# Kernel tuning notes

Measured on AMD Instinct MI355X. Metric: run time of the kernel, lower is better.

## Reference

```python
import jax, jax.numpy as jnp
import numpy as np
from jax import lax

D_MODEL = 200
N_LAYER = 12
NHEADS = 8
HEADDIM = 50
D_STATE = 64
D_INNER = 2 * D_MODEL            # 400
CONV_DIM = D_INNER + 2 * D_STATE  # 528 (ngroups=1)
D_IN_PROJ = 2 * D_INNER + 2 * D_STATE + NHEADS  # 936
D_CONV = 4
EPS = 1e-5


def rmsnorm(x, w):
    v = jnp.mean(jnp.square(x), axis=-1, keepdims=True)
    return x * lax.rsqrt(v + EPS) * w


def groupnorm(x, groups, g, b):
    B, C, H, W = x.shape
    xg = x.reshape(B, groups, C // groups, H, W)
    mu = jnp.mean(xg, axis=(2, 3, 4), keepdims=True)
    var = jnp.mean(jnp.square(xg - mu), axis=(2, 3, 4), keepdims=True)
    xn = ((xg - mu) * lax.rsqrt(var + EPS)).reshape(B, C, H, W)
    return xn * g[:, None, None] + b[:, None, None]


def patch_embed(x, pe_conv_w, proj_in_w, gn_g, gn_b, spec_w):
    b, c, l, d = x.shape
    # time path: 'b c l d' -> (b, 1, c*l, d), conv -> (b, 25, c*l, 8)
    time_x = x.reshape(b, 1, c * l, d)
    t = lax.conv_general_dilated(time_x, proj_in_w, (1, 25), ((0, 0), (24, 24)),
                                 dimension_numbers=('NCHW', 'OIHW', 'NCHW'))
    t = jax.nn.gelu(groupnorm(t, 5, gn_g, gn_b), approximate=False)
    time_emb = t.transpose(0, 2, 1, 3).reshape(b, c, l, D_MODEL)
    # freq path: rfft over patch dim, norm='forward'
    spec = jnp.abs(jnp.fft.rfft(x, axis=-1, norm='forward'))  # (b,c,l,101)
    spec_emb = jnp.einsum('bclf,df->bcld', spec, spec_w)
    patch = time_emb + spec_emb
    # depthwise 7x7 positional conv over (d, c, l)
    pos = lax.conv_general_dilated(patch.transpose(0, 3, 1, 2), pe_conv_w, (1, 1),
                                   ((3, 3), (3, 3)),
                                   dimension_numbers=('NCHW', 'OIHW', 'NCHW'),
                                   feature_group_count=D_MODEL)
    return patch + pos.transpose(0, 2, 3, 1)


def ssd_scan(xh, dt, B, C, A, D):
    # xh: (b,l,h,p)  dt: (b,l,h)  B,C: (b,l,n)  A,D: (h,)
    b, l, h, p = xh.shape

    def step(state, inp):
        x_t, dt_t, B_t, C_t = inp
        dA = jnp.exp(dt_t * A)  # (b,h)
        state = state * dA[:, :, None, None] + \
            (dt_t[:, :, None, None] * x_t[:, :, :, None]) * B_t[:, None, None, :]
        y = jnp.einsum('bhpn,bn->bhp', state, C_t)
        return state, y

    state0 = jnp.zeros((b, h, p, D_STATE), xh.dtype)
    _, ys = lax.scan(step, state0,
                     (xh.transpose(1, 0, 2, 3), dt.transpose(1, 0, 2),
                      B.transpose(1, 0, 2), C.transpose(1, 0, 2)))
    return ys.transpose(1, 0, 2, 3) + xh * D[None, None, :, None]


def mamba2(u, in_w, conv_w, conv_b, dt_bias, A_log, D, gn_w, out_w):
    b, l, _ = u.shape
    zxbcdt = u @ in_w.T  # (b,l,936)
    z = zxbcdt[..., :D_INNER]
    xBC = zxbcdt[..., D_INNER:D_INNER + CONV_DIM]
    dt = jax.nn.softplus(zxbcdt[..., D_INNER + CONV_DIM:] + dt_bias)  # (b,l,8)
    # causal depthwise conv1d, kernel 4
    xc = lax.conv_general_dilated(xBC.transpose(0, 2, 1), conv_w, (1,), ((D_CONV - 1, 0),),
                                  dimension_numbers=('NCH', 'OIH', 'NCH'),
                                  feature_group_count=CONV_DIM)
    xBC = jax.nn.silu((xc + conv_b[:, None]).transpose(0, 2, 1))
    x = xBC[..., :D_INNER].reshape(b, l, NHEADS, HEADDIM)
    Bm = xBC[..., D_INNER:D_INNER + D_STATE]
    Cm = xBC[..., D_INNER + D_STATE:]
    y = ssd_scan(x, dt, Bm, Cm, -jnp.exp(A_log), D).reshape(b, l, D_INNER)
    y = rmsnorm(y * jax.nn.silu(z), gn_w)  # RMSNormGated, norm_before_gate=False
    return y @ out_w.T


@jax.checkpoint
def layer(hidden, residual, norm_w, in_w, conv_w, conv_b, dt_bias, A_log, D, gn_w, out_w):
    residual = hidden + residual
    hidden = mamba2(rmsnorm(residual, norm_w), in_w, conv_w, conv_b, dt_bias, A_log, D, gn_w, out_w)
    return hidden, residual


def forward(x, pe_conv_w, proj_in_w, gn_g, gn_b, spec_w, norm_w, in_proj_w, conv_w, conv_b,
            dt_bias, A_log, D, gnorm_w, out_proj_w, norm_f_w, head_w, head_b):
    b, c, l, d = x.shape
    hidden = patch_embed(x, pe_conv_w, proj_in_w, gn_g, gn_b, spec_w).reshape(b, c * l, d)
    residual = jnp.zeros_like(hidden)
    for i in range(N_LAYER):
        hidden, residual = layer(hidden, residual, norm_w[i], in_proj_w[i], conv_w[i],
                                 conv_b[i], dt_bias[i], A_log[i], D[i], gnorm_w[i], out_proj_w[i])
    hidden = rmsnorm(hidden + residual, norm_f_w).reshape(b, c, l, d)
    return hidden @ head_w.T + head_b


def setup_inputs():
    key = jax.random.key(0)
    ks = jax.random.split(key, 12)
    B, CH, L, P = 16, 19, 30, 200

    def g(k, shape, scale):
        return jax.random.normal(k, shape, jnp.float32) * scale

    dt = jax.random.uniform(ks[8], (N_LAYER, NHEADS), jnp.float32, 1e-3, 0.1)
    return {
        'x': g(ks[0], (B, CH, L, P), 1.0),
        'pe_conv_w': g(ks[1], (D_MODEL, 1, 7, 7), 0.15),
        'proj_in_w': g(ks[2], (25, 1, 1, 49), 0.14),
        'gn_g': jnp.ones(25, jnp.float32),
        'gn_b': jnp.zeros(25, jnp.float32),
        'spec_w': g(ks[3], (D_MODEL, 101), 0.1),
        'norm_w': jnp.ones((N_LAYER, D_MODEL), jnp.float32),
        'in_proj_w': g(ks[4], (N_LAYER, D_IN_PROJ, D_MODEL), 0.07),
        'conv_w': g(ks[5], (N_LAYER, CONV_DIM, 1, D_CONV), 0.4),
        'conv_b': jnp.zeros((N_LAYER, CONV_DIM), jnp.float32),
        'dt_bias': jnp.log(jnp.expm1(dt)),
        'A_log': jnp.log(jax.random.uniform(ks[9], (N_LAYER, NHEADS), jnp.float32, 1.0, 16.0)),
        'D': jnp.ones((N_LAYER, NHEADS), jnp.float32),
        'gnorm_w': jnp.ones((N_LAYER, D_INNER), jnp.float32),
        'out_proj_w': g(ks[6], (N_LAYER, D_MODEL, D_INNER), 0.05),
        'norm_f_w': jnp.ones(D_MODEL, jnp.float32),
        'head_w': g(ks[7], (D_MODEL, D_MODEL), 0.07),
        'head_b': jnp.zeros(D_MODEL, jnp.float32),
    }


def reference(x, pe_conv_w, proj_in_w, gn_g, gn_b, spec_w, norm_w, in_proj_w, conv_w, conv_b,
              dt_bias, A_log, D, gnorm_w, out_proj_w, norm_f_w, head_w, head_b):
    return forward(x, pe_conv_w, proj_in_w, gn_g, gn_b, spec_w, norm_w, in_proj_w, conv_w,
                   conv_b, dt_bias, A_log, D, gnorm_w, out_proj_w, norm_f_w, head_w, head_b)
```

## Files before the change

### kernel.cpp

```cpp
#include <hip/hip_runtime.h>
#include <hip/hip_bf16.h>
#include <math.h>

#define D_MODEL   200
#define N_LAYER   12
#define NHEADS    8
#define HEADDIM   50
#define D_STATE   64
#define D_INNER   400
#define CONV_DIM  528
#define D_IN_PROJ 936
#define D_CONV    4
#define EPS       1e-5f

#define BATCH 16
#define CH    19
#define LLEN  30
#define SEQ   570
#define NTOK  9120
#define NFREQ 101

typedef __attribute__((ext_vector_type(8))) short s8v;
typedef __attribute__((ext_vector_type(4))) float f32x4;

// ... 418 lines not shown
        dtb[(size_t)m * NHEADS + h] = (raw > 20.f) ? raw : log1pf(expf(raw));
    }
}

__global__ __launch_bounds__(256) void dt_gemv_kernel(
    const float* __restrict__ u, const float* __restrict__ Win,
    const float* __restrict__ dt_bias, float* __restrict__ dtb, int layer)
{
    int tid = threadIdx.x;
    int tok = blockIdx.x * 4 + (tid >> 6);
    int head = (tid >> 3) & 7;
    int l8 = tid & 7;
    const float* ur = u + (size_t)tok * 200;
    const float* wr = Win + (size_t)layer * D_IN_PROJ * 200 + (size_t)(928 + head) * 200;
    float s = 0.f;
    for (int k = l8; k < 200; k += 8) s = fmaf(ur[k], wr[k], s);
    s += __shfl_xor(s, 1, 64);
    s += __shfl_xor(s, 2, 64);
    s += __shfl_xor(s, 4, 64);
    if (l8 == 0) {
        float raw = s + dt_bias[layer * NHEADS + head];
        dtb[(size_t)tok * NHEADS + head] = (raw > 20.f) ? raw : log1pf(expf(raw));
    }
}

__global__ __launch_bounds__(256) void dtconv2_kernel(
    const float* __restrict__ zxbcdt, const float* __restrict__ cw,
    const float* __restrict__ cb, float* __restrict__ xBC, int layer)
{
    int b = blockIdx.x, tt = blockIdx.y;
    int t0 = tt * 8;
    __shared__ float zs[11][528];
    const float* cwl = cw + (size_t)layer * CONV_DIM * 4;
    const float* cbl = cb + (size_t)layer * CONV_DIM;
    for (int i = threadIdx.x; i < 11 * 528; i += 256) {
        int r = i / 528, ch = i - r * 528;
        int t = t0 - 3 + r;
        zs[r][ch] = (t >= 0 && t < SEQ)
                        ? zxbcdt[(size_t)(b * SEQ + t) * D_IN_PROJ + D_INNER + ch] : 0.f;
    }
    __syncthreads();
    for (int o = threadIdx.x; o < 8 * 528; o += 256) {
        int tr = o / 528, ch = o - tr * 528;
        int t = t0 + tr;
        if (t >= SEQ) continue;
        float acc = cbl[ch];
#pragma unroll
        for (int k = 0; k < 4; k++)
            acc = fmaf(zs[tr + k][ch], cwl[ch * 4 + k], acc);
        xBC[(size_t)(b * SEQ + t) * CONV_DIM + ch] = acc / (1.f + __expf(-acc));
    }
}

__global__ __launch_bounds__(256) void ssd_state7_kernel(
    const float* __restrict__ xBC, const float* __restrict__ dtb,
    const float* __restrict__ A_log, float* __restrict__ Sbuf,
    float* __restrict__ Pd, int layer, int lchunk, int nchunk)
{
    int b = blockIdx.x, c = blockIdx.y, bz = blockIdx.z;
    int tid = threadIdx.x;
    int hl = tid >> 6, p = tid & 63;
    int h = bz * 4 + hl;
    float A = -expf(A_log[layer * NHEADS + h]);

    __shared__ __align__(16) float sB[4][2][128];
    int t0 = c * lchunk;
    int npairs = lchunk >> 1;

    const float* xb  = xBC + (size_t)(b * SEQ + t0) * CONV_DIM;
    const float* dtp = dtb + (size_t)(b * SEQ + t0) * NHEADS + h;

    int ldtok = (p >> 4) & 1;
    int ldf4  = 100 + (p & 15);
    int ldoff = ldtok * 64 + ((p & 15) << 2);

    float4 gv;
    if (p < 32) {
        gv = ((const float4*)(xb + (size_t)ldtok * CONV_DIM))[ldf4];
        *(float4*)&sB[hl][0][ldoff] = gv;
    }
    float nx0 = (p < HEADDIM) ? xb[h * HEADDIM + p] : 0.f;
    float nx1 = (p < HEADDIM) ? xb[CONV_DIM + h * HEADDIM + p] : 0.f;
    float ndt0 = dtp[0];
    float ndt1 = dtp[NHEADS];
    if (npairs > 1 && p < 32)
        gv = ((const float4*)(xb + (size_t)(2 + ldtok) * CONV_DIM))[ldf4];

    float s[64];
#pragma unroll
    for (int n = 0; n < 64; n++) s[n] = 0.f;
    float pacc = 1.f;

    for (int i = 0; i < npairs; i++) {
        int buf = i & 1;
        float x0 = nx0, x1 = nx1, dt0 = ndt0, dt1 = ndt1;
        if (i + 1 < npairs) {
            if (p < 32) *(float4*)&sB[hl][buf ^ 1][ldoff] = gv;
            const float* xn = xb + (size_t)(2 * (i + 1)) * CONV_DIM;
            nx0 = (p < HEADDIM) ? xn[h * HEADDIM + p] : 0.f;
            nx1 = (p < HEADDIM) ? xn[CONV_DIM + h * HEADDIM + p] : 0.f;
            ndt0 = dtp[(size_t)(2 * (i + 1)) * NHEADS];
            ndt1 = dtp[(size_t)(2 * (i + 1) + 1) * NHEADS];
            if (i + 2 < npairs && p < 32)
                gv = ((const float4*)(xb + (size_t)(2 * (i + 2) + ldtok) * CONV_DIM))[ldf4];
        }
#pragma unroll
        for (int k = 0; k < 2; k++) {
            float dtv = k ? dt1 : dt0;
            float xp  = k ? x1 : x0;
            float dA = __expf(dtv * A);
            float u  = dtv * xp;
            pacc *= dA;
            const float4* B4 = (const float4*)&sB[hl][buf][k * 64];
#pragma unroll
            for (int n4 = 0; n4 < 16; n4++) {
                float4 bq = B4[n4];
                s[4 * n4 + 0] = fmaf(s[4 * n4 + 0], dA, u * bq.x);
                s[4 * n4 + 1] = fmaf(s[4 * n4 + 1], dA, u * bq.y);
                s[4 * n4 + 2] = fmaf(s[4 * n4 + 2], dA, u * bq.z);
                s[4 * n4 + 3] = fmaf(s[4 * n4 + 3], dA, u * bq.w);
            }
        }
    }

    if (p < HEADDIM) {
        float* Sb = Sbuf + ((size_t)((b * NHEADS + h) * nchunk + c)) * (HEADDIM * 64)
                    + p * 64;
#pragma unroll
        for (int n4 = 0; n4 < 16; n4++)
            ((float4*)Sb)[n4] = make_float4(s[4 * n4], s[4 * n4 + 1],
                                            s[4 * n4 + 2], s[4 * n4 + 3]);
    }
    if (p == 0) Pd[(b * NHEADS + h) * nchunk + c] = pacc;
}

__global__ __launch_bounds__(512) void ssd_state_kernel(
    const float* __restrict__ xBC, const float* __restrict__ dtb,
    const float* __restrict__ A_log, float* __restrict__ Sbuf,
    float* __restrict__ Pd, int layer, int lchunk, int nchunk)
{
    int b = blockIdx.x, c = blockIdx.y;
    int tid = threadIdx.x;
    int h = tid >> 6, p = tid & 63;
    float A = -expf(A_log[layer * NHEADS + h]);

    __shared__ float sh[2][544];
    int t0 = c * lchunk, tend = t0 + lchunk;

    {
        const float* base = xBC + (size_t)(b * SEQ + t0) * CONV_DIM;
        sh[0][tid] = base[tid];
        if (tid < 24) {
            int e2 = 512 + tid;
            sh[0][e2] = (e2 < 528) ? base[e2]
                                   : dtb[(size_t)(b * SEQ + t0) * NHEADS + (e2 - 528)];
        }
    }
    __syncthreads();

    float s[64];
#pragma unroll
    for (int n = 0; n < 64; n++) s[n] = 0.f;
    float pacc = 1.f;

    for (int t = t0; t < tend; t++) {
        int cur = (t - t0) & 1, nxt = cur ^ 1;
        float pf0 = 0.f, pf1 = 0.f;
        if (t + 1 < tend) {
            const float* base = xBC + (size_t)(b * SEQ + t + 1) * CONV_DIM;
            pf0 = base[tid];
            if (tid < 24) {
                int e2 = 512 + tid;
                pf1 = (e2 < 528) ? base[e2]
                                 : dtb[(size_t)(b * SEQ + t + 1) * NHEADS + (e2 - 528)];
            }
        }
        float dtv = sh[cur][528 + h];
        float xp  = (p < HEADDIM) ? sh[cur][h * HEADDIM + p] : 0.f;
        float dA = __expf(dtv * A);
        float u  = dtv * xp;
        pacc *= dA;
        const float4* B4 = (const float4*)&sh[cur][D_INNER];
#pragma unroll
        for (int n4 = 0; n4 < 16; n4++) {
            float4 bq = B4[n4];
            s[4 * n4 + 0] = fmaf(s[4 * n4 + 0], dA, u * bq.x);
            s[4 * n4 + 1] = fmaf(s[4 * n4 + 1], dA, u * bq.y);
            s[4 * n4 + 2] = fmaf(s[4 * n4 + 2], dA, u * bq.z);
            s[4 * n4 + 3] = fmaf(s[4 * n4 + 3], dA, u * bq.w);
        }
        if (t + 1 < tend) {
            sh[nxt][tid] = pf0;
            if (tid < 24) sh[nxt][512 + tid] = pf1;
        }
        __syncthreads();
    }

    if (p < HEADDIM) {
        float* Sb = Sbuf + ((size_t)((b * NHEADS + h) * nchunk + c)) * (HEADDIM * 64)
                    + p * 64;
#pragma unroll
        for (int n4 = 0; n4 < 16; n4++)
            ((float4*)Sb)[n4] = make_float4(s[4 * n4], s[4 * n4 + 1],
                                            s[4 * n4 + 2], s[4 * n4 + 3]);
    }
    if (p == 0) Pd[(b * NHEADS + h) * nchunk + c] = pacc;
}

__global__ __launch_bounds__(256) void ssd_scan2b_kernel(
    float* __restrict__ Sbuf, const float* __restrict__ Pd, int nchunk)
{
    int bh = blockIdx.x;
    int e = blockIdx.y * 256 + threadIdx.x;
    if (e >= HEADDIM * 64) return;
    float* base = Sbuf + (size_t)bh * nchunk * (HEADDIM * 64) + e;
    const float* pd = Pd + bh * nchunk;
    float cur = 0.f;
    for (int c = 0; c < nchunk; c++) {
        float l = base[(size_t)c * (HEADDIM * 64)];
        base[(size_t)c * (HEADDIM * 64)] = cur;
        cur = fmaf(pd[c], cur, l);
    }
}

__global__ __launch_bounds__(256) void ssd_out7_kernel(
    const float* __restrict__ xBC, const float* __restrict__ dtb,
    const float* __restrict__ zxbcdt, const float* __restrict__ A_log,
    const float* __restrict__ Dv, const float* __restrict__ Sbuf,
    const float* __restrict__ gw, short* __restrict__ ybf,
    float* __restrict__ ssq, int layer, int lchunk, int nchunk)
{
    int b = blockIdx.x, c = blockIdx.y, bz = blockIdx.z;
    int tid = threadIdx.x;
    int hl = tid >> 6, p = tid & 63;
    int h = bz * 4 + hl;
    float A = -expf(A_log[layer * NHEADS + h]);
    float Dh = Dv[layer * NHEADS + h];
    float gval = (p < HEADDIM) ? gw[(size_t)layer * D_INNER + h * HEADDIM + p] : 0.f;

    __shared__ __align__(16) float sBC[4][2][256];
    int t0 = c * lchunk;
    int npairs = lchunk >> 1;

    const float* xb  = xBC + (size_t)(b * SEQ + t0) * CONV_DIM;
    const float* zb  = zxbcdt + (size_t)(b * SEQ + t0) * D_IN_PROJ;
    const float* dtp = dtb + (size_t)(b * SEQ + t0) * NHEADS + h;

    int ldtok = p >> 5;
    int ldf4  = 100 + (p & 31);
    int ldoff = ldtok * 128 + ((p & 31) << 2);

    float4 gv;
    gv = ((const float4*)(xb + (size_t)ldtok * CONV_DIM))[ldf4];
    *(float4*)&sBC[hl][0][ldoff] = gv;
    float nx0 = (p < HEADDIM) ? xb[h * HEADDIM + p] : 0.f;
    float nx1 = (p < HEADDIM) ? xb[CONV_DIM + h * HEADDIM + p] : 0.f;
    float nz0 = (p < HEADDIM) ? zb[h * HEADDIM + p] : 0.f;
    float nz1 = (p < HEADDIM) ? zb[D_IN_PROJ + h * HEADDIM + p] : 0.f;
    float ndt0 = dtp[0];
    float ndt1 = dtp[NHEADS];
    if (npairs > 1)
        gv = ((const float4*)(xb + (size_t)(2 + ldtok) * CONV_DIM))[ldf4];

    float s[64];
    if (p < HEADDIM) {
        const float* Sb = Sbuf + ((size_t)((b * NHEADS + h) * nchunk + c)) * (HEADDIM * 64)
                          + p * 64;
#pragma unroll
        for (int n4 = 0; n4 < 16; n4++) {
            float4 v = ((const float4*)Sb)[n4];
            s[4 * n4] = v.x; s[4 * n4 + 1] = v.y; s[4 * n4 + 2] = v.z; s[4 * n4 + 3] = v.w;
        }
    } else {
#pragma unroll
        for (int n = 0; n < 64; n++) s[n] = 0.f;
    }

    for (int i = 0; i < npairs; i++) {
        int buf = i & 1;
        int t = t0 + 2 * i;
        float x0 = nx0, x1 = nx1, z0 = nz0, z1 = nz1, dt0 = ndt0, dt1 = ndt1;
        if (i + 1 < npairs) {
            *(float4*)&sBC[hl][buf ^ 1][ldoff] = gv;
            const float* xn = xb + (size_t)(2 * (i + 1)) * CONV_DIM;
            const float* zn = zb + (size_t)(2 * (i + 1)) * D_IN_PROJ;
            nx0 = (p < HEADDIM) ? xn[h * HEADDIM + p] : 0.f;
            nx1 = (p < HEADDIM) ? xn[CONV_DIM + h * HEADDIM + p] : 0.f;
            nz0 = (p < HEADDIM) ? zn[h * HEADDIM + p] : 0.f;
            nz1 = (p < HEADDIM) ? zn[D_IN_PROJ + h * HEADDIM + p] : 0.f;
            ndt0 = dtp[(size_t)(2 * (i + 1)) * NHEADS];
            ndt1 = dtp[(size_t)(2 * (i + 1) + 1) * NHEADS];
            if (i + 2 < npairs)
                gv = ((const float4*)(xb + (size_t)(2 * (i + 2) + ldtok) * CONV_DIM))[ldf4];
        }
#pragma unroll
        for (int k = 0; k < 2; k++) {
            float dtv = k ? dt1 : dt0;
            float xp  = k ? x1 : x0;
            float zv  = k ? z1 : z0;
            float dA = __expf(dtv * A);
            float u  = dtv * xp;
            const float4* B4 = (const float4*)&sBC[hl][buf][k * 128];
            const float4* C4 = (const float4*)&sBC[hl][buf][k * 128 + 64];
            float y0 = 0.f, y1 = 0.f, y2 = 0.f, y3 = 0.f;
#pragma unroll
            for (int n4 = 0; n4 < 16; n4++) {
                float4 bq = B4[n4];
                float4 cq = C4[n4];
                float t0v = fmaf(s[4 * n4 + 0], dA, u * bq.x);
                float t1v = fmaf(s[4 * n4 + 1], dA, u * bq.y);
                float t2v = fmaf(s[4 * n4 + 2], dA, u * bq.z);
                float t3v = fmaf(s[4 * n4 + 3], dA, u * bq.w);
                s[4 * n4 + 0] = t0v; s[4 * n4 + 1] = t1v;
                s[4 * n4 + 2] = t2v; s[4 * n4 + 3] = t3v;
                y0 = fmaf(t0v, cq.x, y0);
                y1 = fmaf(t1v, cq.y, y1);
                y2 = fmaf(t2v, cq.z, y2);
                y3 = fmaf(t3v, cq.w, y3);
            }
            float g0 = 0.f;
            if (p < HEADDIM) {
                float yv = fmaf(xp, Dh, (y0 + y1) + (y2 + y3));
                g0 = yv * (zv / (1.f + __expf(-zv)));
            }
            size_t row0 = (size_t)(b * SEQ + t + k) * 416;
            if (p < HEADDIM) {
                ybf[row0 + h * HEADDIM + p] = f2bf(g0 * gval);
            } else {
                int widx = h * 14 + (p - HEADDIM);
                if (widx < 16) ybf[row0 + 400 + widx] = 0;
            }
            float gs0 = g0 * g0;
#pragma unroll
            for (int o = 32; o; o >>= 1) gs0 += __shfl_xor(gs0, o, 64);
            if (p == 0) ssq[(size_t)(b * SEQ + t + k) * NHEADS + h] = gs0;
        }
    }
}

__global__ __launch_bounds__(256) void rstd_kernel(
    const float* __restrict__ ssq, float* __restrict__ rstdb)
{
    int m = blockIdx.x * 256 + threadIdx.x;
    if (m >= NTOK) return;
    const float4* q = (const float4*)(ssq + (size_t)m * NHEADS);
    float4 a = q[0], bq = q[1];
    float tot = ((a.x + a.y) + (a.z + a.w)) + ((bq.x + bq.y) + (bq.z + bq.w));
    rstdb[m] = rsqrtf(tot * (1.f / D_INNER) + EPS);
}

__global__ __launch_bounds__(512) void ssd_out_kernel(
    const float* __restrict__ xBC, const float* __restrict__ dtb,
    const float* __restrict__ A_log, const float* __restrict__ Dv,
    const float* __restrict__ Sbuf, float* __restrict__ y,
    int layer, int lchunk, int nchunk)
{
    int b = blockIdx.x, c = blockIdx.y;
    int tid = threadIdx.x;
    int h = tid >> 6, p = tid & 63;
    float A = -expf(A_log[layer * NHEADS + h]);
    float Dh = Dv[layer * NHEADS + h];

    __shared__ float sh[2][544];
    int t0 = c * lchunk, tend = t0 + lchunk;

    {
        const float* base = xBC + (size_t)(b * SEQ + t0) * CONV_DIM;
        sh[0][tid] = base[tid];
        if (tid < 24) {
            int e2 = 512 + tid;
            sh[0][e2] = (e2 < 528) ? base[e2]
                                   : dtb[(size_t)(b * SEQ + t0) * NHEADS + (e2 - 528)];
        }
    }

    float s[64];
    if (p < HEADDIM) {
        const float* Sb = Sbuf + ((size_t)((b * NHEADS + h) * nchunk + c)) * (HEADDIM * 64)
                          + p * 64;
#pragma unroll
        for (int n4 = 0; n4 < 16; n4++) {
            float4 v = ((const float4*)Sb)[n4];
            s[4 * n4] = v.x; s[4 * n4 + 1] = v.y; s[4 * n4 + 2] = v.z; s[4 * n4 + 3] = v.w;
        }
    } else {
#pragma unroll
        for (int n = 0; n < 64; n++) s[n] = 0.f;
    }
    __syncthreads();
// ... 55 lines not shown
    float* yr = y + (size_t)m * D_INNER;
    const float* gwl = gw + (size_t)layer * D_INNER;
    float ss = 0.f;
    for (int k = threadIdx.x; k < D_INNER; k += 256) {
        float zv = z[k];
        float sz = zv / (1.f + expf(-zv));
        float g = yr[k] * sz;
        buf[k] = g;
        ss = fmaf(g, g, ss);
    }
    int lane = threadIdx.x & 63, w = threadIdx.x >> 6;
#pragma unroll
    for (int o = 32; o; o >>= 1) ss += __shfl_xor(ss, o, 64);
    if (lane == 0) red[w] = ss;
    __syncthreads();
    float tot = red[0] + red[1] + red[2] + red[3];
    float rstd = rsqrtf(tot * (1.f / D_INNER) + EPS);
    for (int k = threadIdx.x; k < 416; k += 256) {
        if (k < D_INNER) {
            float v = buf[k] * rstd * gwl[k];
            yr[k] = v;
            if (ybf) ybf[(size_t)m * 416 + k] = f2bf(v);
        } else if (ybf) {
            ybf[(size_t)m * 416 + k] = 0;
        }
    }
}

extern "C" void kernel_launch(void* const* d_in, const int* in_sizes, int n_in,
                              void* d_out, int out_size, void* d_ws, size_t ws_size,
                              hipStream_t stream)
{
    const float* x         = (const float*)d_in[0];
    const float* pe_conv_w = (const float*)d_in[1];
    const float* proj_in_w = (const float*)d_in[2];
    const float* gn_g      = (const float*)d_in[3];
    const float* gn_b      = (const float*)d_in[4];
    const float* spec_w    = (const float*)d_in[5];
    const float* norm_w    = (const float*)d_in[6];
    const float* in_proj_w = (const float*)d_in[7];
    const float* conv_w    = (const float*)d_in[8];
    const float* conv_b    = (const float*)d_in[9];
    const float* dt_bias   = (const float*)d_in[10];
    const float* A_log     = (const float*)d_in[11];
    const float* Dv        = (const float*)d_in[12];
    const float* gnorm_w   = (const float*)d_in[13];
    const float* out_proj_w= (const float*)d_in[14];
    const float* norm_f_w  = (const float*)d_in[15];
    const float* head_w    = (const float*)d_in[16];
    const float* head_b    = (const float*)d_in[17];
    float* out = (float*)d_out;
    float* ws  = (float*)d_ws;

    const size_t needA = 28011424ull * sizeof(float);
    int fast = (ws_size >= needA) ? 1 : 0;

    int nchunk, lchunk;
    float *residual = ws, *hidden = ws + 1824000;
    float *zxbcdt, *xBC, *dtb, *Sbuf, *Pd;
    float *ubuf = nullptr, *ybuf = nullptr, *ssq = nullptr, *rstdb = nullptr;
    short *w_in_bf = nullptr, *w_out_bf = nullptr, *w_head_bf = nullptr,
          *w_spec_bf = nullptr, *csmat_bf = nullptr, *x_bf = nullptr,
          *ubuf_bf = nullptr, *ybuf_bf = nullptr, *magb_bf = nullptr;

    if (fast) {
        nchunk = 15; lchunk = 38;
        zxbcdt = ws + 3648000;
        xBC    = ws + 12184320;
        dtb    = ws + 16999680;
        Sbuf   = ws + 17072640;
        Pd     = ws + 23216640;
        short* pool = (short*)(ws + 23218560);
        w_in_bf   = pool;
        w_out_bf  = pool + 2515968;
        w_head_bf = pool + 3514368;
        w_spec_bf = pool + 3559168;
        ubuf_bf   = pool + 3584768;
        ybuf_bf   = pool + 5627648;
        ssq       = ws + 27929344;
        rstdb     = ws + 28002304;
        csmat_bf  = (short*)(Sbuf + 4000000);
        x_bf      = (short*)(Sbuf + 4100000);
        magb_bf   = (short*)(Sbuf + 5200000);
    } else {
        nchunk = 6; lchunk = 95;
        ubuf   = ws + 3648000;
        zxbcdt = ws + 5472000;
        xBC    = ws + 14008320;
        dtb    = ws + 18823680;
        ybuf   = ws + 18896640;
        Sbuf   = ws + 1824000;
        Pd     = ws + 5470000;
    }

    float* traw  = fast ? Sbuf : ybuf;
    float* patch = zxbcdt;
    float* csout = fast ? (Sbuf + 2000000) : (xBC + 50000);
    float* csmat = xBC;
    float* magb  = fast ? nullptr : (xBC + 2000000);
    float* stats = dtb;

    if (fast) {
        cast_pad_kernel<<<(12 * 936 * 224 + 255) / 256, 256, 0, stream>>>(
            in_proj_w, w_in_bf, 12 * 936, 200, 224);
        cast_pad_kernel<<<(12 * 200 * 416 + 255) / 256, 256, 0, stream>>>(
            out_proj_w, w_out_bf, 12 * 200, 400, 416);
        cast_pad_kernel<<<(200 * 224 + 255) / 256, 256, 0, stream>>>(
            head_w, w_head_bf, 200, 200, 224);
        cast_pad_kernel<<<(200 * 128 + 255) / 256, 256, 0, stream>>>(
            spec_w, w_spec_bf, 200, 101, 128);
        cast_pad_kernel<<<(9120 * 224 + 255) / 256, 256, 0, stream>>>(
            x, x_bf, 9120, 200, 224);
        dft_init_bf_kernel<<<(202 * 224 + 255) / 256, 256, 0, stream>>>(csmat_bf);
    } else {
        dft_init_kernel<<<(202 * 200 + 255) / 256, 256, 0, stream>>>(csmat);
    }

    time_conv_kernel<<<NTOK, 256, 0, stream>>>(x, proj_in_w, traw);
    gn_stats_kernel<<<80, 256, 0, stream>>>(traw, stats);
    gn_gelu_kernel<<<(NTOK * 200 + 255) / 256, 256, 0, stream>>>(traw, stats, gn_g, gn_b, patch);
    if (fast) {
        gemm_bf16<<<dim3(2, 72), 256, 0, stream>>>(x_bf, csmat_bf, nullptr, nullptr, csout,
                                                   NTOK, 202, 224, 0);
        mag_bf_kernel<<<(NTOK * 128 + 255) / 256, 256, 0, stream>>>(csout, magb_bf);
        gemm_bf16<<<dim3(2, 72), 256, 0, stream>>>(magb_bf, w_spec_bf, nullptr, nullptr, patch,
                                                   NTOK, 200, 128, 1);
    } else {
        gemm_nt<<<dim3(2, 72), 256, 0, stream>>>(x, csmat, nullptr, csout, NTOK, 202, 200, 0);
        mag_kernel<<<(NTOK * NFREQ + 255) / 256, 256, 0, stream>>>(csout, magb);
        gemm_nt<<<dim3(2, 72), 256, 0, stream>>>(magb, spec_w, nullptr, patch,
                                                 NTOK, 200, NFREQ, 1);
    }
    pe_conv3_kernel<<<dim3(16, 13, 5), 256, 0, stream>>>(patch, pe_conv_w, hidden);

    for (int i = 0; i < N_LAYER; i++) {
        if (fast) {
            norm_dt_kernel<<<NTOK, 256, 0, stream>>>(hidden, residual, norm_w + i * 200,
                                                     ubuf_bf, in_proj_w, dt_bias, dtb,
                                                     i, (i == 0) ? 1 : 0);
            gemm_bf16<<<dim3(8, 72), 256, 0, stream>>>(
                ubuf_bf, w_in_bf + (size_t)i * 936 * 224, nullptr, nullptr, zxbcdt,
                NTOK, D_IN_PROJ, 224, 0);
        } else {
            add_rmsnorm_kernel<<<NTOK, 64, 0, stream>>>(hidden, residual, norm_w + i * 200,
                                                        ubuf, nullptr, (i == 0) ? 1 : 0);
            dt_gemv_kernel<<<NTOK / 4, 256, 0, stream>>>(ubuf, in_proj_w, dt_bias, dtb, i);
            gemm_nt<<<dim3(8, 72), 256, 0, stream>>>(
                ubuf, in_proj_w + (size_t)i * D_IN_PROJ * 200, nullptr, zxbcdt,
                NTOK, D_IN_PROJ, 200, 0);
        }
        dtconv2_kernel<<<dim3(16, 72), 256, 0, stream>>>(zxbcdt, conv_w, conv_b, xBC, i);
        {
            dim3 g(BATCH, nchunk);
            if (fast) {
                ssd_state7_kernel<<<dim3(BATCH, nchunk, 2), 256, 0, stream>>>(
                    xBC, dtb, A_log, Sbuf, Pd, i, lchunk, nchunk);
                ssd_scan2b_kernel<<<dim3(BATCH * NHEADS, 13), 256, 0, stream>>>(Sbuf, Pd, nchunk);
                ssd_out7_kernel<<<dim3(BATCH, nchunk, 2), 256, 0, stream>>>(
                    xBC, dtb, zxbcdt, A_log, Dv, Sbuf, gnorm_w, ybuf_bf, ssq,
                    i, lchunk, nchunk);
                rstd_kernel<<<(NTOK + 255) / 256, 256, 0, stream>>>(ssq, rstdb);
                gemm_bf16<<<dim3(2, 72), 256, 0, stream>>>(
                    ybuf_bf, w_out_bf + (size_t)i * 200 * 416, nullptr, rstdb, hidden,
                    NTOK, 200, 416, 0);
            } else {
                ssd_state_kernel<<<g, 512, 0, stream>>>(xBC, dtb, A_log, Sbuf, Pd,
                                                        i, lchunk, nchunk);
                ssd_scan2b_kernel<<<dim3(BATCH * NHEADS, 13), 256, 0, stream>>>(Sbuf, Pd, nchunk);
                ssd_out_kernel<<<g, 512, 0, stream>>>(xBC, dtb, A_log, Dv, Sbuf, ybuf,
                                                      i, lchunk, nchunk);
                gate_norm_kernel<<<NTOK, 256, 0, stream>>>(ybuf, zxbcdt, gnorm_w, nullptr, i);
                gemm_nt<<<dim3(2, 72), 256, 0, stream>>>(
                    ybuf, out_proj_w + (size_t)i * 200 * D_INNER, nullptr, hidden,
                    NTOK, 200, D_INNER, 0);
            }
        }
    }

    add_rmsnorm_kernel<<<NTOK, 64, 0, stream>>>(hidden, residual, norm_f_w,
                                                fast ? nullptr : ubuf,
                                                fast ? ubuf_bf : nullptr, 0);
    if (fast) {
        gemm_bf16<<<dim3(2, 72), 256, 0, stream>>>(ubuf_bf, w_head_bf, head_b, nullptr, out,
                                                   NTOK, 200, 224, 0);
    } else {
        gemm_nt<<<dim3(2, 72), 256, 0, stream>>>(ubuf, head_w, head_b, out,
                                                 NTOK, 200, 200, 0);
    }
}
```

Measured before the change: 2.441 ms.

## Restructure chunked SSD scan into single recurrence pass plus lightweight correction

The state pass now runs the full intra-chunk recurrence starting from a zero state. In the same pass it emits the chunk-local output (including the D skip term) and the running decay product per token to new buffers. A new fix kernel then adds the inter-chunk contribution Pt·(C·S_prev) and applies gating, the bf16 store and the sum-of-squares, with no second sequential recurrence. This avoids redoing the whole state recurrence in the output kernel, at the cost of extra global traffic for yraw/ptb and a larger workspace requirement.

```diff
diff --git a/kernel.cpp b/kernel.cpp
--- a/kernel.cpp
+++ b/kernel.cpp
@@ -494,38 +494,39 @@
     }
 }
 
-__global__ __launch_bounds__(256) void ssd_state7_kernel(
+__global__ __launch_bounds__(256) void ssd_scan9_kernel(
     const float* __restrict__ xBC, const float* __restrict__ dtb,
-    const float* __restrict__ A_log, float* __restrict__ Sbuf,
-    float* __restrict__ Pd, int layer, int lchunk, int nchunk)
+    const float* __restrict__ A_log, const float* __restrict__ Dv,
+    float* __restrict__ Sbuf, float* __restrict__ Pd,
+    float* __restrict__ ptb, float* __restrict__ yraw,
+    int layer, int lchunk, int nchunk)
 {
     int b = blockIdx.x, c = blockIdx.y, bz = blockIdx.z;
     int tid = threadIdx.x;
     int hl = tid >> 6, p = tid & 63;
     int h = bz * 4 + hl;
     float A = -expf(A_log[layer * NHEADS + h]);
-
-    __shared__ __align__(16) float sB[4][2][128];
+    float Dh = Dv[layer * NHEADS + h];
+
+    __shared__ __align__(16) float sBC[4][2][256];
     int t0 = c * lchunk;
     int npairs = lchunk >> 1;
 
     const float* xb  = xBC + (size_t)(b * SEQ + t0) * CONV_DIM;
     const float* dtp = dtb + (size_t)(b * SEQ + t0) * NHEADS + h;
 
-    int ldtok = (p >> 4) & 1;
-    int ldf4  = 100 + (p & 15);
-    int ldoff = ldtok * 64 + ((p & 15) << 2);
+    int ldtok = p >> 5;
+    int ldf4  = 100 + (p & 31);
+    int ldoff = ldtok * 128 + ((p & 31) << 2);
 
     float4 gv;
-    if (p < 32) {
-        gv = ((const float4*)(xb + (size_t)ldtok * CONV_DIM))[ldf4];
-        *(float4*)&sB[hl][0][ldoff] = gv;
-    }
+    gv = ((const float4*)(xb + (size_t)ldtok * CONV_DIM))[ldf4];
+    *(float4*)&sBC[hl][0][ldoff] = gv;
     float nx0 = (p < HEADDIM) ? xb[h * HEADDIM + p] : 0.f;
     float nx1 = (p < HEADDIM) ? xb[CONV_DIM + h * HEADDIM + p] : 0.f;
     float ndt0 = dtp[0];
     float ndt1 = dtp[NHEADS];
-    if (npairs > 1 && p < 32)
+    if (npairs > 1)
         gv = ((const float4*)(xb + (size_t)(2 + ldtok) * CONV_DIM))[ldf4];
 
     float s[64];
@@ -535,15 +536,16 @@
 
     for (int i = 0; i < npairs; i++) {
         int buf = i & 1;
+        int t = t0 + 2 * i;
         float x0 = nx0, x1 = nx1, dt0 = ndt0, dt1 = ndt1;
         if (i + 1 < npairs) {
-            if (p < 32) *(float4*)&sB[hl][buf ^ 1][ldoff] = gv;
+            *(float4*)&sBC[hl][buf ^ 1][ldoff] = gv;
             const float* xn = xb + (size_t)(2 * (i + 1)) * CONV_DIM;
             nx0 = (p < HEADDIM) ? xn[h * HEADDIM + p] : 0.f;
             nx1 = (p < HEADDIM) ? xn[CONV_DIM + h * HEADDIM + p] : 0.f;
             ndt0 = dtp[(size_t)(2 * (i + 1)) * NHEADS];
             ndt1 = dtp[(size_t)(2 * (i + 1) + 1) * NHEADS];
-            if (i + 2 < npairs && p < 32)
+            if (i + 2 < npairs)
                 gv = ((const float4*)(xb + (size_t)(2 * (i + 2) + ldtok) * CONV_DIM))[ldf4];
         }
 #pragma unroll
@@ -553,195 +555,6 @@
             float dA = __expf(dtv * A);
             float u  = dtv * xp;
             pacc *= dA;
-            const float4* B4 = (const float4*)&sB[hl][buf][k * 64];
-#pragma unroll
-            for (int n4 = 0; n4 < 16; n4++) {
-                float4 bq = B4[n4];
-                s[4 * n4 + 0] = fmaf(s[4 * n4 + 0], dA, u * bq.x);
-                s[4 * n4 + 1] = fmaf(s[4 * n4 + 1], dA, u * bq.y);
-                s[4 * n4 + 2] = fmaf(s[4 * n4 + 2], dA, u * bq.z);
-                s[4 * n4 + 3] = fmaf(s[4 * n4 + 3], dA, u * bq.w);
-            }
-        }
-    }
-
-    if (p < HEADDIM) {
-        float* Sb = Sbuf + ((size_t)((b * NHEADS + h) * nchunk + c)) * (HEADDIM * 64)
-                    + p * 64;
-#pragma unroll
-        for (int n4 = 0; n4 < 16; n4++)
-            ((float4*)Sb)[n4] = make_float4(s[4 * n4], s[4 * n4 + 1],
-                                            s[4 * n4 + 2], s[4 * n4 + 3]);
-    }
-    if (p == 0) Pd[(b * NHEADS + h) * nchunk + c] = pacc;
-}
-
-__global__ __launch_bounds__(512) void ssd_state_kernel(
-    const float* __restrict__ xBC, const float* __restrict__ dtb,
-    const float* __restrict__ A_log, float* __restrict__ Sbuf,
-    float* __restrict__ Pd, int layer, int lchunk, int nchunk)
-{
-    int b = blockIdx.x, c = blockIdx.y;
-    int tid = threadIdx.x;
-    int h = tid >> 6, p = tid & 63;
-    float A = -expf(A_log[layer * NHEADS + h]);
-
-    __shared__ float sh[2][544];
-    int t0 = c * lchunk, tend = t0 + lchunk;
-
-    {
-        const float* base = xBC + (size_t)(b * SEQ + t0) * CONV_DIM;
-        sh[0][tid] = base[tid];
-        if (tid < 24) {
-            int e2 = 512 + tid;
-            sh[0][e2] = (e2 < 528) ? base[e2]
-                                   : dtb[(size_t)(b * SEQ + t0) * NHEADS + (e2 - 528)];
-        }
-    }
-    __syncthreads();
-
-    float s[64];
-#pragma unroll
-    for (int n = 0; n < 64; n++) s[n] = 0.f;
-    float pacc = 1.f;
-
-    for (int t = t0; t < tend; t++) {
-        int cur = (t - t0) & 1, nxt = cur ^ 1;
-        float pf0 = 0.f, pf1 = 0.f;
-        if (t + 1 < tend) {
-            const float* base = xBC + (size_t)(b * SEQ + t + 1) * CONV_DIM;
-            pf0 = base[tid];
-            if (tid < 24) {
-                int e2 = 512 + tid;
-                pf1 = (e2 < 528) ? base[e2]
-                                 : dtb[(size_t)(b * SEQ + t + 1) * NHEADS + (e2 - 528)];
-            }
-        }
-        float dtv = sh[cur][528 + h];
-        float xp  = (p < HEADDIM) ? sh[cur][h * HEADDIM + p] : 0.f;
-        float dA = __expf(dtv * A);
-        float u  = dtv * xp;
-        pacc *= dA;
-        const float4* B4 = (const float4*)&sh[cur][D_INNER];
-#pragma unroll
-        for (int n4 = 0; n4 < 16; n4++) {
-            float4 bq = B4[n4];
-            s[4 * n4 + 0] = fmaf(s[4 * n4 + 0], dA, u * bq.x);
-            s[4 * n4 + 1] = fmaf(s[4 * n4 + 1], dA, u * bq.y);
-            s[4 * n4 + 2] = fmaf(s[4 * n4 + 2], dA, u * bq.z);
-            s[4 * n4 + 3] = fmaf(s[4 * n4 + 3], dA, u * bq.w);
-        }
-        if (t + 1 < tend) {
-            sh[nxt][tid] = pf0;
-            if (tid < 24) sh[nxt][512 + tid] = pf1;
-        }
-        __syncthreads();
-    }
-
-    if (p < HEADDIM) {
-        float* Sb = Sbuf + ((size_t)((b * NHEADS + h) * nchunk + c)) * (HEADDIM * 64)
-                    + p * 64;
-#pragma unroll
-        for (int n4 = 0; n4 < 16; n4++)
-            ((float4*)Sb)[n4] = make_float4(s[4 * n4], s[4 * n4 + 1],
-                                            s[4 * n4 + 2], s[4 * n4 + 3]);
-    }
-    if (p == 0) Pd[(b * NHEADS + h) * nchunk + c] = pacc;
-}
-
-__global__ __launch_bounds__(256) void ssd_scan2b_kernel(
-    float* __restrict__ Sbuf, const float* __restrict__ Pd, int nchunk)
-{
-    int bh = blockIdx.x;
-    int e = blockIdx.y * 256 + threadIdx.x;
-    if (e >= HEADDIM * 64) return;
-    float* base = Sbuf + (size_t)bh * nchunk * (HEADDIM * 64) + e;
-    const float* pd = Pd + bh * nchunk;
-    float cur = 0.f;
-    for (int c = 0; c < nchunk; c++) {
-        float l = base[(size_t)c * (HEADDIM * 64)];
-        base[(size_t)c * (HEADDIM * 64)] = cur;
-        cur = fmaf(pd[c], cur, l);
-    }
-}
-
-__global__ __launch_bounds__(256) void ssd_out7_kernel(
-    const float* __restrict__ xBC, const float* __restrict__ dtb,
-    const float* __restrict__ zxbcdt, const float* __restrict__ A_log,
-    const float* __restrict__ Dv, const float* __restrict__ Sbuf,
-    const float* __restrict__ gw, short* __restrict__ ybf,
-    float* __restrict__ ssq, int layer, int lchunk, int nchunk)
-{
-    int b = blockIdx.x, c = blockIdx.y, bz = blockIdx.z;
-    int tid = threadIdx.x;
-    int hl = tid >> 6, p = tid & 63;
-    int h = bz * 4 + hl;
-    float A = -expf(A_log[layer * NHEADS + h]);
-    float Dh = Dv[layer * NHEADS + h];
-    float gval = (p < HEADDIM) ? gw[(size_t)layer * D_INNER + h * HEADDIM + p] : 0.f;
-
-    __shared__ __align__(16) float sBC[4][2][256];
-    int t0 = c * lchunk;
-    int npairs = lchunk >> 1;
-
-    const float* xb  = xBC + (size_t)(b * SEQ + t0) * CONV_DIM;
-    const float* zb  = zxbcdt + (size_t)(b * SEQ + t0) * D_IN_PROJ;
-    const float* dtp = dtb + (size_t)(b * SEQ + t0) * NHEADS + h;
-
-    int ldtok = p >> 5;
-    int ldf4  = 100 + (p & 31);
-    int ldoff = ldtok * 128 + ((p & 31) << 2);
-
-    float4 gv;
-    gv = ((const float4*)(xb + (size_t)ldtok * CONV_DIM))[ldf4];
-    *(float4*)&sBC[hl][0][ldoff] = gv;
-    float nx0 = (p < HEADDIM) ? xb[h * HEADDIM + p] : 0.f;
-    float nx1 = (p < HEADDIM) ? xb[CONV_DIM + h * HEADDIM + p] : 0.f;
-    float nz0 = (p < HEADDIM) ? zb[h * HEADDIM + p] : 0.f;
-    float nz1 = (p < HEADDIM) ? zb[D_IN_PROJ + h * HEADDIM + p] : 0.f;
-    float ndt0 = dtp[0];
-    float ndt1 = dtp[NHEADS];
-    if (npairs > 1)
-        gv = ((const float4*)(xb + (size_t)(2 + ldtok) * CONV_DIM))[ldf4];
-
-    float s[64];
-    if (p < HEADDIM) {
-        const float* Sb = Sbuf + ((size_t)((b * NHEADS + h) * nchunk + c)) * (HEADDIM * 64)
-                          + p * 64;
-#pragma unroll
-        for (int n4 = 0; n4 < 16; n4++) {
-            float4 v = ((const float4*)Sb)[n4];
-            s[4 * n4] = v.x; s[4 * n4 + 1] = v.y; s[4 * n4 + 2] = v.z; s[4 * n4 + 3] = v.w;
-        }
-    } else {
-#pragma unroll
-        for (int n = 0; n < 64; n++) s[n] = 0.f;
-    }
-
-    for (int i = 0; i < npairs; i++) {
-        int buf = i & 1;
-        int t = t0 + 2 * i;
-        float x0 = nx0, x1 = nx1, z0 = nz0, z1 = nz1, dt0 = ndt0, dt1 = ndt1;
-        if (i + 1 < npairs) {
-            *(float4*)&sBC[hl][buf ^ 1][ldoff] = gv;
-            const float* xn = xb + (size_t)(2 * (i + 1)) * CONV_DIM;
-            const float* zn = zb + (size_t)(2 * (i + 1)) * D_IN_PROJ;
-            nx0 = (p < HEADDIM) ? xn[h * HEADDIM + p] : 0.f;
-            nx1 = (p < HEADDIM) ? xn[CONV_DIM + h * HEADDIM + p] : 0.f;
-            nz0 = (p < HEADDIM) ? zn[h * HEADDIM + p] : 0.f;
-            nz1 = (p < HEADDIM) ? zn[D_IN_PROJ + h * HEADDIM + p] : 0.f;
-            ndt0 = dtp[(size_t)(2 * (i + 1)) * NHEADS];
-            ndt1 = dtp[(size_t)(2 * (i + 1) + 1) * NHEADS];
-            if (i + 2 < npairs)
-                gv = ((const float4*)(xb + (size_t)(2 * (i + 2) + ldtok) * CONV_DIM))[ldf4];
-        }
-#pragma unroll
-        for (int k = 0; k < 2; k++) {
-            float dtv = k ? dt1 : dt0;
-            float xp  = k ? x1 : x0;
-            float zv  = k ? z1 : z0;
-            float dA = __expf(dtv * A);
-            float u  = dtv * xp;
             const float4* B4 = (const float4*)&sBC[hl][buf][k * 128];
             const float4* C4 = (const float4*)&sBC[hl][buf][k * 128 + 64];
             float y0 = 0.f, y1 = 0.f, y2 = 0.f, y3 = 0.f;
@@ -760,23 +573,178 @@
                 y2 = fmaf(t2v, cq.z, y2);
                 y3 = fmaf(t3v, cq.w, y3);
             }
-            float g0 = 0.f;
-            if (p < HEADDIM) {
-                float yv = fmaf(xp, Dh, (y0 + y1) + (y2 + y3));
-                g0 = yv * (zv / (1.f + __expf(-zv)));
+            if (p < HEADDIM)
+                yraw[(size_t)(b * SEQ + t + k) * D_INNER + h * HEADDIM + p]
+                    = fmaf(xp, Dh, (y0 + y1) + (y2 + y3));
+            if (p == 0)
+                ptb[(size_t)(b * SEQ + t + k) * NHEADS + h] = pacc;
+        }
+    }
+
+    if (p < HEADDIM) {
+        float* Sb = Sbuf + ((size_t)((b * NHEADS + h) * nchunk + c)) * (HEADDIM * 64)
+                    + p * 64;
+#pragma unroll
+        for (int n4 = 0; n4 < 16; n4++)
+            ((float4*)Sb)[n4] = make_float4(s[4 * n4], s[4 * n4 + 1],
+                                            s[4 * n4 + 2], s[4 * n4 + 3]);
+    }
+    if (p == 0) Pd[(b * NHEADS + h) * nchunk + c] = pacc;
+}
+
+__global__ __launch_bounds__(512) void ssd_state_kernel(
+    const float* __restrict__ xBC, const float* __restrict__ dtb,
+    const float* __restrict__ A_log, float* __restrict__ Sbuf,
+    float* __restrict__ Pd, int layer, int lchunk, int nchunk)
+{
+    int b = blockIdx.x, c = blockIdx.y;
+    int tid = threadIdx.x;
+    int h = tid >> 6, p = tid & 63;
+    float A = -expf(A_log[layer * NHEADS + h]);
+
+    __shared__ float sh[2][544];
+    int t0 = c * lchunk, tend = t0 + lchunk;
+
+    {
+        const float* base = xBC + (size_t)(b * SEQ + t0) * CONV_DIM;
+        sh[0][tid] = base[tid];
+        if (tid < 24) {
+            int e2 = 512 + tid;
+            sh[0][e2] = (e2 < 528) ? base[e2]
+                                   : dtb[(size_t)(b * SEQ + t0) * NHEADS + (e2 - 528)];
+        }
+    }
+    __syncthreads();
+
+    float s[64];
+#pragma unroll
+    for (int n = 0; n < 64; n++) s[n] = 0.f;
+    float pacc = 1.f;
+
+    for (int t = t0; t < tend; t++) {
+        int cur = (t - t0) & 1, nxt = cur ^ 1;
+        float pf0 = 0.f, pf1 = 0.f;
+        if (t + 1 < tend) {
+            const float* base = xBC + (size_t)(b * SEQ + t + 1) * CONV_DIM;
+            pf0 = base[tid];
+            if (tid < 24) {
+                int e2 = 512 + tid;
+                pf1 = (e2 < 528) ? base[e2]
+                                 : dtb[(size_t)(b * SEQ + t + 1) * NHEADS + (e2 - 528)];
             }
-            size_t row0 = (size_t)(b * SEQ + t + k) * 416;
-            if (p < HEADDIM) {
-                ybf[row0 + h * HEADDIM + p] = f2bf(g0 * gval);
-            } else {
-                int widx = h * 14 + (p - HEADDIM);
-                if (widx < 16) ybf[row0 + 400 + widx] = 0;
-            }
-            float gs0 = g0 * g0;
-#pragma unroll
-            for (int o = 32; o; o >>= 1) gs0 += __shfl_xor(gs0, o, 64);
-            if (p == 0) ssq[(size_t)(b * SEQ + t + k) * NHEADS + h] = gs0;
-        }
+        }
+        float dtv = sh[cur][528 + h];
+        float xp  = (p < HEADDIM) ? sh[cur][h * HEADDIM + p] : 0.f;
+        float dA = __expf(dtv * A);
+        float u  = dtv * xp;
+        pacc *= dA;
+        const float4* B4 = (const float4*)&sh[cur][D_INNER];
+#pragma unroll
+        for (int n4 = 0; n4 < 16; n4++) {
+            float4 bq = B4[n4];
+            s[4 * n4 + 0] = fmaf(s[4 * n4 + 0], dA, u * bq.x);
+            s[4 * n4 + 1] = fmaf(s[4 * n4 + 1], dA, u * bq.y);
+            s[4 * n4 + 2] = fmaf(s[4 * n4 + 2], dA, u * bq.z);
+            s[4 * n4 + 3] = fmaf(s[4 * n4 + 3], dA, u * bq.w);
+        }
+        if (t + 1 < tend) {
+            sh[nxt][tid] = pf0;
+            if (tid < 24) sh[nxt][512 + tid] = pf1;
+        }
+        __syncthreads();
+    }
+
+    if (p < HEADDIM) {
+        float* Sb = Sbuf + ((size_t)((b * NHEADS + h) * nchunk + c)) * (HEADDIM * 64)
+                    + p * 64;
+#pragma unroll
+        for (int n4 = 0; n4 < 16; n4++)
+            ((float4*)Sb)[n4] = make_float4(s[4 * n4], s[4 * n4 + 1],
+                                            s[4 * n4 + 2], s[4 * n4 + 3]);
+    }
+    if (p == 0) Pd[(b * NHEADS + h) * nchunk + c] = pacc;
+}
+
+__global__ __launch_bounds__(256) void ssd_scan2b_kernel(
+    float* __restrict__ Sbuf, const float* __restrict__ Pd, int nchunk)
+{
+    int bh = blockIdx.x;
+    int e = blockIdx.y * 256 + threadIdx.x;
+    if (e >= HEADDIM * 64) return;
+    float* base = Sbuf + (size_t)bh * nchunk * (HEADDIM * 64) + e;
+    const float* pd = Pd + bh * nchunk;
+    float cur = 0.f;
+    for (int c = 0; c < nchunk; c++) {
+        float l = base[(size_t)c * (HEADDIM * 64)];
+        base[(size_t)c * (HEADDIM * 64)] = cur;
+        cur = fmaf(pd[c], cur, l);
+    }
+}
+
+__global__ __launch_bounds__(256) void ssd_fix9_kernel(
+    const float* __restrict__ xBC, const float* __restrict__ zxbcdt,
+    const float* __restrict__ Sbuf, const float* __restrict__ ptb,
+    const float* __restrict__ yraw, const float* __restrict__ gw,
+    short* __restrict__ ybf, float* __restrict__ ssq,
+    int layer, int lchunk, int nchunk)
+{
+    int b = blockIdx.x, c = blockIdx.y, bz = blockIdx.z;
+    int tid = threadIdx.x;
+    int hl = tid >> 6, p = tid & 63;
+    int h = bz * 4 + hl;
+    float gval = (p < HEADDIM) ? gw[(size_t)layer * D_INNER + h * HEADDIM + p] : 0.f;
+
+    int t0 = c * lchunk;
+    float s[64];
+    if (p < HEADDIM) {
+        const float* Sb = Sbuf + ((size_t)((b * NHEADS + h) * nchunk + c)) * (HEADDIM * 64)
+                          + p * 64;
+#pragma unroll
+        for (int n4 = 0; n4 < 16; n4++) {
+            float4 v = ((const float4*)Sb)[n4];
+            s[4 * n4] = v.x; s[4 * n4 + 1] = v.y; s[4 * n4 + 2] = v.z; s[4 * n4 + 3] = v.w;
+        }
+    } else {
+#pragma unroll
+        for (int n = 0; n < 64; n++) s[n] = 0.f;
+    }
+
+    const float* xb = xBC + (size_t)(b * SEQ + t0) * CONV_DIM;
+    const float* zb = zxbcdt + (size_t)(b * SEQ + t0) * D_IN_PROJ;
+
+    for (int t = 0; t < lchunk; t++) {
+        size_t m = (size_t)(b * SEQ + t0 + t);
+        float Pt = ptb[m * NHEADS + h];
+        float zv = (p < HEADDIM) ? zb[h * HEADDIM + p] : 0.f;
+        float yr = (p < HEADDIM) ? yraw[m * D_INNER + h * HEADDIM + p] : 0.f;
+        const float4* C4 = (const float4*)(xb + D_INNER + D_STATE);
+        float y0 = 0.f, y1 = 0.f, y2 = 0.f, y3 = 0.f;
+#pragma unroll
+        for (int n4 = 0; n4 < 16; n4++) {
+            float4 cq = C4[n4];
+            y0 = fmaf(s[4 * n4 + 0], cq.x, y0);
+            y1 = fmaf(s[4 * n4 + 1], cq.y, y1);
+            y2 = fmaf(s[4 * n4 + 2], cq.z, y2);
+            y3 = fmaf(s[4 * n4 + 3], cq.w, y3);
+        }
+        float g0 = 0.f;
+        if (p < HEADDIM) {
+            float y = fmaf(Pt, (y0 + y1) + (y2 + y3), yr);
+            g0 = y * (zv / (1.f + __expf(-zv)));
+        }
+        size_t row0 = m * 416;
+        if (p < HEADDIM) {
+            ybf[row0 + h * HEADDIM + p] = f2bf(g0 * gval);
+        } else {
+            int widx = h * 14 + (p - HEADDIM);
+            if (widx < 16) ybf[row0 + 400 + widx] = 0;
+        }
+        float gs0 = g0 * g0;
+#pragma unroll
+        for (int o = 32; o; o >>= 1) gs0 += __shfl_xor(gs0, o, 64);
+        if (p == 0) ssq[m * NHEADS + h] = gs0;
+        xb += CONV_DIM;
+        zb += D_IN_PROJ;
     }
 }
 
@@ -938,13 +906,14 @@
     float* out = (float*)d_out;
     float* ws  = (float*)d_ws;
 
-    const size_t needA = 28011424ull * sizeof(float);
+    const size_t needA = 31732384ull * sizeof(float);
     int fast = (ws_size >= needA) ? 1 : 0;
 
     int nchunk, lchunk;
     float *residual = ws, *hidden = ws + 1824000;
     float *zxbcdt, *xBC, *dtb, *Sbuf, *Pd;
     float *ubuf = nullptr, *ybuf = nullptr, *ssq = nullptr, *rstdb = nullptr;
+    float *ptb = nullptr, *yraw = nullptr;
     short *w_in_bf = nullptr, *w_out_bf = nullptr, *w_head_bf = nullptr,
           *w_spec_bf = nullptr, *csmat_bf = nullptr, *x_bf = nullptr,
           *ubuf_bf = nullptr, *ybuf_bf = nullptr, *magb_bf = nullptr;
@@ -965,6 +934,8 @@
         ybuf_bf   = pool + 5627648;
         ssq       = ws + 27929344;
         rstdb     = ws + 28002304;
+        ptb       = ws + 28011424;
+        yraw      = ws + 28084384;
         csmat_bf  = (short*)(Sbuf + 4000000);
         x_bf      = (short*)(Sbuf + 4100000);
         magb_bf   = (short*)(Sbuf + 5200000);
@@ -1039,11 +1010,11 @@
         {
             dim3 g(BATCH, nchunk);
             if (fast) {
-                ssd_state7_kernel<<<dim3(BATCH, nchunk, 2), 256, 0, stream>>>(
-                    xBC, dtb, A_log, Sbuf, Pd, i, lchunk, nchunk);
+                ssd_scan9_kernel<<<dim3(BATCH, nchunk, 2), 256, 0, stream>>>(
+                    xBC, dtb, A_log, Dv, Sbuf, Pd, ptb, yraw, i, lchunk, nchunk);
                 ssd_scan2b_kernel<<<dim3(BATCH * NHEADS, 13), 256, 0, stream>>>(Sbuf, Pd, nchunk);
-                ssd_out7_kernel<<<dim3(BATCH, nchunk, 2), 256, 0, stream>>>(
-                    xBC, dtb, zxbcdt, A_log, Dv, Sbuf, gnorm_w, ybuf_bf, ssq,
+                ssd_fix9_kernel<<<dim3(BATCH, nchunk, 2), 256, 0, stream>>>(
+                    xBC, zxbcdt, Sbuf, ptb, yraw, gnorm_w, ybuf_bf, ssq,
                     i, lchunk, nchunk);
                 rstd_kernel<<<(NTOK + 255) / 256, 256, 0, stream>>>(ssq, rstdb);
                 gemm_bf16<<<dim3(2, 72), 256, 0, stream>>>(
```

New measurement: 2.762 ms. 1.13x slower.

## Compute SSD chunk states via bf16 MFMA with prefix-sum decay weights

Applied to the files above, without the earlier changes.

Replaces the sequential per-token recurrence in the chunk-state kernel with a closed form. A wave-level prefix sum of dt*A gives the decay weights, the decay-weighted X and B are staged as bf16 in shared memory, and the state is computed as a 64x64 matrix product on MFMA instructions. This removes the serial token loop and its dependent FMA chain. In exchange it drops state-computation inputs to bf16 precision and assumes lchunk is at most 64.

```diff
diff --git a/kernel.cpp b/kernel.cpp
--- a/kernel.cpp
+++ b/kernel.cpp
@@ -494,86 +494,91 @@
     }
 }
 
-__global__ __launch_bounds__(256) void ssd_state7_kernel(
+__global__ __launch_bounds__(256) void ssd_state12_kernel(
     const float* __restrict__ xBC, const float* __restrict__ dtb,
     const float* __restrict__ A_log, float* __restrict__ Sbuf,
     float* __restrict__ Pd, int layer, int lchunk, int nchunk)
 {
     int b = blockIdx.x, c = blockIdx.y, bz = blockIdx.z;
     int tid = threadIdx.x;
-    int hl = tid >> 6, p = tid & 63;
-    int h = bz * 4 + hl;
+    int w = tid >> 6, lane = tid & 63;
+    int h = bz * 4 + w;
+    int t0 = c * lchunk;
     float A = -expf(A_log[layer * NHEADS + h]);
 
-    __shared__ __align__(16) float sB[4][2][128];
-    int t0 = c * lchunk;
-    int npairs = lchunk >> 1;
-
-    const float* xb  = xBC + (size_t)(b * SEQ + t0) * CONV_DIM;
-    const float* dtp = dtb + (size_t)(b * SEQ + t0) * NHEADS + h;
-
-    int ldtok = (p >> 4) & 1;
-    int ldf4  = 100 + (p & 15);
-    int ldoff = ldtok * 64 + ((p & 15) << 2);
-
-    float4 gv;
-    if (p < 32) {
-        gv = ((const float4*)(xb + (size_t)ldtok * CONV_DIM))[ldf4];
-        *(float4*)&sB[hl][0][ldoff] = gv;
-    }
-    float nx0 = (p < HEADDIM) ? xb[h * HEADDIM + p] : 0.f;
-    float nx1 = (p < HEADDIM) ? xb[CONV_DIM + h * HEADDIM + p] : 0.f;
-    float ndt0 = dtp[0];
-    float ndt1 = dtp[NHEADS];
-    if (npairs > 1 && p < 32)
-        gv = ((const float4*)(xb + (size_t)(2 + ldtok) * CONV_DIM))[ldf4];
-
-    float s[64];
-#pragma unroll
-    for (int n = 0; n < 64; n++) s[n] = 0.f;
-    float pacc = 1.f;
-
-    for (int i = 0; i < npairs; i++) {
-        int buf = i & 1;
-        float x0 = nx0, x1 = nx1, dt0 = ndt0, dt1 = ndt1;
-        if (i + 1 < npairs) {
-            if (p < 32) *(float4*)&sB[hl][buf ^ 1][ldoff] = gv;
-            const float* xn = xb + (size_t)(2 * (i + 1)) * CONV_DIM;
-            nx0 = (p < HEADDIM) ? xn[h * HEADDIM + p] : 0.f;
-            nx1 = (p < HEADDIM) ? xn[CONV_DIM + h * HEADDIM + p] : 0.f;
-            ndt0 = dtp[(size_t)(2 * (i + 1)) * NHEADS];
-            ndt1 = dtp[(size_t)(2 * (i + 1) + 1) * NHEADS];
-            if (i + 2 < npairs && p < 32)
-                gv = ((const float4*)(xb + (size_t)(2 * (i + 2) + ldtok) * CONV_DIM))[ldf4];
-        }
-#pragma unroll
-        for (int k = 0; k < 2; k++) {
-            float dtv = k ? dt1 : dt0;
-            float xp  = k ? x1 : x0;
-            float dA = __expf(dtv * A);
-            float u  = dtv * xp;
-            pacc *= dA;
-            const float4* B4 = (const float4*)&sB[hl][buf][k * 64];
-#pragma unroll
-            for (int n4 = 0; n4 < 16; n4++) {
-                float4 bq = B4[n4];
-                s[4 * n4 + 0] = fmaf(s[4 * n4 + 0], dA, u * bq.x);
-                s[4 * n4 + 1] = fmaf(s[4 * n4 + 1], dA, u * bq.y);
-                s[4 * n4 + 2] = fmaf(s[4 * n4 + 2], dA, u * bq.z);
-                s[4 * n4 + 3] = fmaf(s[4 * n4 + 3], dA, u * bq.w);
+    __shared__ __align__(16) short Bt[64 * 64];
+    __shared__ __align__(16) short Xw[4][64 * 64];
+
+    for (int i = tid; i < 512; i += 256) ((s8v*)Bt)[i] = (s8v)0;
+#pragma unroll
+    for (int ww = 0; ww < 4; ww++)
+        for (int i = tid; i < 512; i += 256) ((s8v*)Xw[ww])[i] = (s8v)0;
+    __syncthreads();
+
+    float dtv = 0.f;
+    if (lane < lchunk) dtv = dtb[(size_t)(b * SEQ + t0 + lane) * NHEADS + h];
+    float lc = dtv * A;
+#pragma unroll
+    for (int o = 1; o < 64; o <<= 1) {
+        float v = __shfl_up(lc, o, 64);
+        if (lane >= o) lc += v;
+    }
+    float lcTot = __shfl(lc, lchunk - 1, 64);
+    float wdec = __expf(lcTot - lc) * dtv;
+
+    for (int idx = tid; idx < lchunk * 64; idx += 256) {
+        int s = idx >> 6, n = idx & 63;
+        float v = xBC[(size_t)(b * SEQ + t0 + s) * CONV_DIM + D_INNER + n];
+        Bt[n * 64 + s] = f2bf(v);
+    }
+    for (int idx = lane; idx < lchunk * HEADDIM; idx += 64) {
+        int s = idx / HEADDIM, p = idx - s * HEADDIM;
+        float ws = __shfl(wdec, s, 64);
+        float v = xBC[(size_t)(b * SEQ + t0 + s) * CONV_DIM + h * HEADDIM + p] * ws;
+        Xw[w][p * 64 + s] = f2bf(v);
+    }
+    __syncthreads();
+
+    int lm = lane & 15, lg = lane >> 4;
+    f32x4 acc[4][4];
+#pragma unroll
+    for (int i = 0; i < 4; i++)
+#pragma unroll
+        for (int j = 0; j < 4; j++) acc[i][j] = (f32x4)0.f;
+
+#pragma unroll
+    for (int k0 = 0; k0 < 64; k0 += 32) {
+        s8v af[4], bf[4];
+#pragma unroll
+        for (int i = 0; i < 4; i++)
+            af[i] = *(const s8v*)&Xw[w][(i * 16 + lm) * 64 + k0 + lg * 8];
+#pragma unroll
+        for (int j = 0; j < 4; j++)
+            bf[j] = *(const s8v*)&Bt[(j * 16 + lm) * 64 + k0 + lg * 8];
+#pragma unroll
+        for (int i = 0; i < 4; i++)
+#pragma unroll
+            for (int j = 0; j < 4; j++)
+                acc[i][j] = __builtin_amdgcn_mfma_f32_16x16x32_bf16(
+                    af[i], bf[j], acc[i][j], 0, 0, 0);
+    }
+
+    float* Sb = Sbuf + ((size_t)((b * NHEADS + h) * nchunk + c)) * (HEADDIM * 64);
+#pragma unroll
+    for (int i = 0; i < 4; i++) {
+        int pbase = i * 16 + lg * 4;
+#pragma unroll
+        for (int r = 0; r < 4; r++) {
+            int p = pbase + r;
+            if (p >= HEADDIM) continue;
+#pragma unroll
+            for (int j = 0; j < 4; j++) {
+                int n = j * 16 + lm;
+                Sb[(size_t)p * 64 + n] = acc[i][j][r];
             }
         }
     }
-
-    if (p < HEADDIM) {
-        float* Sb = Sbuf + ((size_t)((b * NHEADS + h) * nchunk + c)) * (HEADDIM * 64)
-                    + p * 64;
-#pragma unroll
-        for (int n4 = 0; n4 < 16; n4++)
-            ((float4*)Sb)[n4] = make_float4(s[4 * n4], s[4 * n4 + 1],
-                                            s[4 * n4 + 2], s[4 * n4 + 3]);
-    }
-    if (p == 0) Pd[(b * NHEADS + h) * nchunk + c] = pacc;
+    if (lane == 0) Pd[(b * NHEADS + h) * nchunk + c] = __expf(lcTot);
 }
 
 __global__ __launch_bounds__(512) void ssd_state_kernel(
@@ -1039,7 +1044,7 @@
         {
             dim3 g(BATCH, nchunk);
             if (fast) {
-                ssd_state7_kernel<<<dim3(BATCH, nchunk, 2), 256, 0, stream>>>(
+                ssd_state12_kernel<<<dim3(BATCH, nchunk, 2), 256, 0, stream>>>(
                     xBC, dtb, A_log, Sbuf, Pd, i, lchunk, nchunk);
                 ssd_scan2b_kernel<<<dim3(BATCH * NHEADS, 13), 256, 0, stream>>>(Sbuf, Pd, nchunk);
                 ssd_out7_kernel<<<dim3(BATCH, nchunk, 2), 256, 0, stream>>>(
```

After: 2.301 ms. 5.7% less time.
